# Kernel tuning notes

Measured on AMD Instinct MI355X. Metric: run time of the kernel, lower is better.

Reference implementation:

```python
import jax, jax.numpy as jnp
import numpy as np

N, E, B, D, L = 50000, 1600000, 128, 64, 5
BN_EPS = 1e-5

def _bn(x, g, b, m, v):
    # eval-mode BatchNorm1d with running stats
    return (x - m) * jax.lax.rsqrt(v + BN_EPS) * g + b

def setup_inputs() -> dict:
    key = jax.random.key(0)
    ks = iter(jax.random.split(key, 64))
    w = 1.0 / np.sqrt(D)
    def nrm(shape, s):
        return jax.random.normal(next(ks), shape, jnp.float32) * s
    def var(shape):
        return jax.random.uniform(next(ks), shape, jnp.float32) + 0.5
    inp = {
        "x": nrm((N, D), 1.0),
        "lin_W": nrm((D, D), w), "lin_b": nrm((D,), w),
        "eps": jnp.zeros((L,), jnp.float32),
        "gin_W1": nrm((L, D, D), w), "gin_b1": nrm((L, D), w),
        "gin_bn_g": jnp.ones((L, D), jnp.float32), "gin_bn_b": jnp.zeros((L, D), jnp.float32),
        "gin_bn_m": nrm((L, D), 0.1), "gin_bn_v": var((L, D)),
        "gin_W2": nrm((L, D, D), w), "gin_b2": nrm((L, D), w),
        "bn_g": jnp.ones((L, D), jnp.float32), "bn_b": jnp.zeros((L, D), jnp.float32),
        "bn_m": nrm((L, D), 0.1), "bn_v": var((L, D)),
        "vn_emb": jnp.zeros((D,), jnp.float32),  # init constant 0 per source
        "vn_W1": nrm((L - 1, D, D), w), "vn_b1": nrm((L - 1, D), w),
        "vn_bn1_g": jnp.ones((L - 1, D), jnp.float32), "vn_bn1_b": jnp.zeros((L - 1, D), jnp.float32),
        "vn_bn1_m": nrm((L - 1, D), 0.1), "vn_bn1_v": var((L - 1, D)),
        "vn_W2": nrm((L - 1, D, D), w), "vn_b2": nrm((L - 1, D), w),
        "vn_bn2_g": jnp.ones((L - 1, D), jnp.float32), "vn_bn2_b": jnp.zeros((L - 1, D), jnp.float32),
        "vn_bn2_m": nrm((L - 1, D), 0.1), "vn_bn2_v": var((L - 1, D)),
        "src": jax.random.randint(next(ks), (E,), 0, N, jnp.int32),
        "dst": jax.random.randint(next(ks), (E,), 0, N, jnp.int32),
        "batch_id": jnp.sort(jax.random.randint(next(ks), (N,), 0, B, jnp.int32)),
    }
    return inp

def reference(x, lin_W, lin_b, eps, gin_W1, gin_b1, gin_bn_g, gin_bn_b, gin_bn_m, gin_bn_v,
              gin_W2, gin_b2, bn_g, bn_b, bn_m, bn_v, vn_emb,
              vn_W1, vn_b1, vn_bn1_g, vn_bn1_b, vn_bn1_m, vn_bn1_v,
              vn_W2, vn_b2, vn_bn2_g, vn_bn2_b, vn_bn2_m, vn_bn2_v,
              src, dst, batch_id):
    n = x.shape[0]
    h = x @ lin_W + lin_b                       # input linear [N, D]
    h_list = [h]
    vn = jnp.broadcast_to(vn_emb, (B, D))       # per-graph virtual node [B, D]
    for l in range(L):
        h_list[l] = h_list[l] + vn[batch_id]    # virtual-node broadcast to nodes
        hl = h_list[l]
        # GINConv: sum over incoming edges of relu(src feature)
        agg = jax.ops.segment_sum(jax.nn.relu(hl[src]), dst, num_segments=n)
        z = (1.0 + eps[l]) * hl + agg
        z = z @ gin_W1[l] + gin_b1[l]
        z = jax.nn.relu(_bn(z, gin_bn_g[l], gin_bn_b[l], gin_bn_m[l], gin_bn_v[l]))
        z = z @ gin_W2[l] + gin_b2[l]
        z = _bn(z, bn_g[l], bn_b[l], bn_m[l], bn_v[l])  # outer batchnorm
        if l != L - 1:
            z = jax.nn.relu(z)                  # dropout is identity in eval mode
        h_list.append(z)
        if l < L - 1:
            # sum-pool nodes per graph, update virtual node via MLP
            vt = jax.ops.segment_sum(hl, batch_id, num_segments=B) + vn
            vt = vt @ vn_W1[l] + vn_b1[l]
            vt = jax.nn.relu(_bn(vt, vn_bn1_g[l], vn_bn1_b[l], vn_bn1_m[l], vn_bn1_v[l]))
            vt = vt @ vn_W2[l] + vn_b2[l]
            vn = jax.nn.relu(_bn(vt, vn_bn2_g[l], vn_bn2_b[l], vn_bn2_m[l], vn_bn2_v[l]))
    # JK='sum' in the source sums h_list[0..num_layers-1] (excludes final entry)
    out = h_list[0]
    for l in range(1, L):
        out = out + h_list[l]
    return out
```

## Files before the change

kernel.cpp:

```cpp
#include <hip/hip_runtime.h>

#define N_NODES 50000
#define N_EDGES 1600000
#define NB 128
#define GB 782
#define CAP 80
#define NODE_RANGE 6250
#define EDGE_BLOCKS 6250
#define INIT_BLOCKS 32

__device__ __forceinline__ unsigned short f2bf(float f) {
    unsigned u = __float_as_uint(f);
    unsigned r = (u + 0x7FFFu + ((u >> 16) & 1u)) >> 16;
    return (unsigned short)r;
}

__global__ __launch_bounds__(256) void k_build(
    const int* __restrict__ src, const int* __restrict__ dst,
    int* __restrict__ cnt, unsigned short* __restrict__ csr_src,
    const float* __restrict__ vn_emb, float* __restrict__ pooled) {
    int bid = blockIdx.x;
    if (bid >= EDGE_BLOCKS * 8) {
        int t = (bid - EDGE_BLOCKS * 8) * 256 + threadIdx.x;
        pooled[t] = vn_emb[t & 63];
        return;
    }
    int range = bid & 7;
    int e = (bid >> 3) * 256 + threadIdx.x;
    int d = dst[e];
    if (d / NODE_RANGE != range) return;
    int pos = atomicAdd(&cnt[d], 1);
    if (pos < CAP) csr_src[(size_t)d * CAP + pos] = (unsigned short)src[e];
}

__global__ __launch_bounds__(256) void k_lin_pre(
    const float* __restrict__ in, const float* __restrict__ W,
    const float* __restrict__ bias, const float* __restrict__ vn_emb,
    const int* __restrict__ batch_id,
    float* __restrict__ h, float* __restrict__ out,
    unsigned short* __restrict__ rbuf, float* __restrict__ pooled) {
    __shared__ float sW[64 * 64];
    __shared__ float sIn[64 * 68];
    int tid = threadIdx.x;
    int row0 = blockIdx.x * 64;

    const float4* W4 = (const float4*)W;
#pragma unroll
    for (int i = 0; i < 4; ++i) ((float4*)sW)[tid + 256 * i] = W4[tid + 256 * i];
    const float4* in4 = (const float4*)in;
#pragma unroll
    for (int i = 0; i < 4; ++i) {
        int idx = tid + 256 * i;
        int r = idx >> 4, j = idx & 15;
        float4 val = make_float4(0.f, 0.f, 0.f, 0.f);
        if (row0 + r < N_NODES) val = in4[(size_t)(row0 + r) * 16 + j];
        ((float4*)(sIn + r * 68))[j] = val;
    }
    __syncthreads();

    int c4 = (tid & 15) * 4;
    int rl = (tid >> 4) * 4;
    float acc[4][4] = {{0.f}};
#pragma unroll 8
    for (int k = 0; k < 64; ++k) {
        float4 wv = *(const float4*)(sW + k * 64 + c4);
        float a0 = sIn[(rl + 0) * 68 + k];
        float a1 = sIn[(rl + 1) * 68 + k];
        float a2 = sIn[(rl + 2) * 68 + k];
        float a3 = sIn[(rl + 3) * 68 + k];
        acc[0][0] += a0 * wv.x; acc[0][1] += a0 * wv.y; acc[0][2] += a0 * wv.z; acc[0][3] += a0 * wv.w;
        acc[1][0] += a1 * wv.x; acc[1][1] += a1 * wv.y; acc[1][2] += a1 * wv.z; acc[1][3] += a1 * wv.w;
        acc[2][0] += a2 * wv.x; acc[2][1] += a2 * wv.y; acc[2][2] += a2 * wv.z; acc[2][3] += a2 * wv.w;
        acc[3][0] += a3 * wv.x; acc[3][1] += a3 * wv.y; acc[3][2] += a3 * wv.z; acc[3][3] += a3 * wv.w;
    }
    float shf[4];
#pragma unroll
    for (int j = 0; j < 4; ++j) shf[j] = bias[c4 + j] + vn_emb[c4 + j];

    int lane = tid & 63;
    int wave = tid >> 6;
    int wr0 = row0 + wave * 16;
    bool full = (wr0 + 15 < N_NODES);
    bool fast = full && (batch_id[wr0] == batch_id[wr0 + 15]);
    float4 pacc = make_float4(0.f, 0.f, 0.f, 0.f);
#pragma unroll
    for (int r = 0; r < 4; ++r) {
        int row = row0 + rl + r;
        if (row >= N_NODES) continue;
        float4 v;
        v.x = acc[r][0] + shf[0];
        v.y = acc[r][1] + shf[1];
        v.z = acc[r][2] + shf[2];
        v.w = acc[r][3] + shf[3];
        *(float4*)(h + (size_t)row * 64 + c4) = v;
        *(float4*)(out + (size_t)row * 64 + c4) = v;
        ushort4 rb;
        rb.x = f2bf(fmaxf(v.x, 0.f)); rb.y = f2bf(fmaxf(v.y, 0.f));
        rb.z = f2bf(fmaxf(v.z, 0.f)); rb.w = f2bf(fmaxf(v.w, 0.f));
        *(ushort4*)(rbuf + (size_t)row * 64 + c4) = rb;
        if (fast) {
            pacc.x += v.x; pacc.y += v.y; pacc.z += v.z; pacc.w += v.w;
        } else {
            int b = batch_id[row];
            atomicAdd(&pooled[b * 64 + c4 + 0], v.x);
            atomicAdd(&pooled[b * 64 + c4 + 1], v.y);
            atomicAdd(&pooled[b * 64 + c4 + 2], v.z);
            atomicAdd(&pooled[b * 64 + c4 + 3], v.w);
        }
    }
    if (fast) {
        pacc.x += __shfl_xor(pacc.x, 16); pacc.x += __shfl_xor(pacc.x, 32);
        pacc.y += __shfl_xor(pacc.y, 16); pacc.y += __shfl_xor(pacc.y, 32);
        pacc.z += __shfl_xor(pacc.z, 16); pacc.z += __shfl_xor(pacc.z, 32);
        pacc.w += __shfl_xor(pacc.w, 16); pacc.w += __shfl_xor(pacc.w, 32);
        if ((lane >> 4) == 0) {
            int b = batch_id[wr0];
            atomicAdd(&pooled[b * 64 + c4 + 0], pacc.x);
            atomicAdd(&pooled[b * 64 + c4 + 1], pacc.y);
            atomicAdd(&pooled[b * 64 + c4 + 2], pacc.z);
            atomicAdd(&pooled[b * 64 + c4 + 3], pacc.w);
        }
    }
}

__global__ __launch_bounds__(512) void k_gin(
    const float* __restrict__ h_in, const float* __restrict__ eps, int l,
    const int* __restrict__ cnt, const unsigned short* __restrict__ csr_src,
    const unsigned short* __restrict__ rbuf_in,
    const float* __restrict__ W1, const float* __restrict__ b1,
    const float* __restrict__ g1, const float* __restrict__ be1,
    const float* __restrict__ m1, const float* __restrict__ v1,
    const float* __restrict__ W2, const float* __restrict__ b2,
    const float* __restrict__ g2, const float* __restrict__ be2,
    const float* __restrict__ m2, const float* __restrict__ v2,
    const float* __restrict__ vn, const int* __restrict__ batch_id,
    float* __restrict__ h, float* __restrict__ out,
    unsigned short* __restrict__ rbuf_out, float* __restrict__ pooled,
    int last) {
    __shared__ float sW[64 * 64];
    __shared__ float sIn[64 * 68];
    int tid = threadIdx.x;
    int row0 = blockIdx.x * 64;
    int lane = tid & 63;
    int wave = tid >> 6;

#pragma unroll
    for (int i = 0; i < 2; ++i)
        ((float4*)sW)[tid + 512 * i] = ((const float4*)W1)[tid + 512 * i];

    {
        int g = lane >> 3, f4 = lane & 7;
        int row = row0 + wave * 8 + g;
        float e1 = 1.0f + eps[l];
        const uint4* tab4 = (const uint4*)rbuf_in;
        float aL0 = 0.f, aH0 = 0.f, aL1 = 0.f, aH1 = 0.f;
        float aL2 = 0.f, aH2 = 0.f, aL3 = 0.f, aH3 = 0.f;
        if (row < N_NODES) {
            int deg = cnt[row]; if (deg > CAP) deg = CAP;
            const unsigned short* rowp = csr_src + (size_t)row * CAP;
            int e = 0;
            for (; e + 3 < deg; e += 4) {
                ushort4 s4 = *(const ushort4*)(rowp + e);
                uint4 u0 = tab4[(size_t)s4.x * 8 + f4];
                uint4 u1 = tab4[(size_t)s4.y * 8 + f4];
                uint4 u2 = tab4[(size_t)s4.z * 8 + f4];
                uint4 u3 = tab4[(size_t)s4.w * 8 + f4];
                aL0 += __uint_as_float(u0.x << 16); aH0 += __uint_as_float(u0.x & 0xFFFF0000u);
                aL1 += __uint_as_float(u0.y << 16); aH1 += __uint_as_float(u0.y & 0xFFFF0000u);
                aL2 += __uint_as_float(u0.z << 16); aH2 += __uint_as_float(u0.z & 0xFFFF0000u);
                aL3 += __uint_as_float(u0.w << 16); aH3 += __uint_as_float(u0.w & 0xFFFF0000u);
                aL0 += __uint_as_float(u1.x << 16); aH0 += __uint_as_float(u1.x & 0xFFFF0000u);
                aL1 += __uint_as_float(u1.y << 16); aH1 += __uint_as_float(u1.y & 0xFFFF0000u);
                aL2 += __uint_as_float(u1.z << 16); aH2 += __uint_as_float(u1.z & 0xFFFF0000u);
                aL3 += __uint_as_float(u1.w << 16); aH3 += __uint_as_float(u1.w & 0xFFFF0000u);
                aL0 += __uint_as_float(u2.x << 16); aH0 += __uint_as_float(u2.x & 0xFFFF0000u);
                aL1 += __uint_as_float(u2.y << 16); aH1 += __uint_as_float(u2.y & 0xFFFF0000u);
                aL2 += __uint_as_float(u2.z << 16); aH2 += __uint_as_float(u2.z & 0xFFFF0000u);
                aL3 += __uint_as_float(u2.w << 16); aH3 += __uint_as_float(u2.w & 0xFFFF0000u);
                aL0 += __uint_as_float(u3.x << 16); aH0 += __uint_as_float(u3.x & 0xFFFF0000u);
                aL1 += __uint_as_float(u3.y << 16); aH1 += __uint_as_float(u3.y & 0xFFFF0000u);
                aL2 += __uint_as_float(u3.z << 16); aH2 += __uint_as_float(u3.z & 0xFFFF0000u);
                aL3 += __uint_as_float(u3.w << 16); aH3 += __uint_as_float(u3.w & 0xFFFF0000u);
            }
            for (; e < deg; ++e) {
                uint4 u = tab4[(size_t)rowp[e] * 8 + f4];
                aL0 += __uint_as_float(u.x << 16); aH0 += __uint_as_float(u.x & 0xFFFF0000u);
                aL1 += __uint_as_float(u.y << 16); aH1 += __uint_as_float(u.y & 0xFFFF0000u);
                aL2 += __uint_as_float(u.z << 16); aH2 += __uint_as_float(u.z & 0xFFFF0000u);
                aL3 += __uint_as_float(u.w << 16); aH3 += __uint_as_float(u.w & 0xFFFF0000u);
            }
        }
        float* sp = sIn + (wave * 8 + g) * 68 + f4 * 8;
        if (row < N_NODES) {
            const float* hp = h_in + (size_t)row * 64 + f4 * 8;
            float4 h0 = *(const float4*)hp;
            float4 h1 = *(const float4*)(hp + 4);
            float4 o0, o1;
            o0.x = e1 * h0.x + aL0; o0.y = e1 * h0.y + aH0;
            o0.z = e1 * h0.z + aL1; o0.w = e1 * h0.w + aH1;
            o1.x = e1 * h1.x + aL2; o1.y = e1 * h1.y + aH2;
            o1.z = e1 * h1.z + aL3; o1.w = e1 * h1.w + aH3;
            *(float4*)sp = o0;
            *(float4*)(sp + 4) = o1;
        } else {
            *(float4*)sp = make_float4(0.f, 0.f, 0.f, 0.f);
            *(float4*)(sp + 4) = make_float4(0.f, 0.f, 0.f, 0.f);
        }
    }
    __syncthreads();

    int c4 = (tid & 15) * 4;
    int rg = tid >> 4;
    float acc[2][4] = {{0.f}};
#pragma unroll 8
    for (int k = 0; k < 64; ++k) {
        float4 wv = *(const float4*)(sW + k * 64 + c4);
        float a0 = sIn[(2 * rg + 0) * 68 + k];
        float a1 = sIn[(2 * rg + 1) * 68 + k];
        acc[0][0] += a0 * wv.x; acc[0][1] += a0 * wv.y; acc[0][2] += a0 * wv.z; acc[0][3] += a0 * wv.w;
        acc[1][0] += a1 * wv.x; acc[1][1] += a1 * wv.y; acc[1][2] += a1 * wv.z; acc[1][3] += a1 * wv.w;
    }
    float scl[4], shf[4];
#pragma unroll
    for (int j = 0; j < 4; ++j) {
        int c = c4 + j;
        float sc = g1[c] * rsqrtf(v1[c] + 1e-5f);
        scl[j] = sc;
        shf[j] = be1[c] - m1[c] * sc + b1[c] * sc;
    }
    __syncthreads();
#pragma unroll
    for (int i = 0; i < 2; ++i) {
        float4 z;
        z.x = fmaxf(acc[i][0] * scl[0] + shf[0], 0.f);
        z.y = fmaxf(acc[i][1] * scl[1] + shf[1], 0.f);
        z.z = fmaxf(acc[i][2] * scl[2] + shf[2], 0.f);
        z.w = fmaxf(acc[i][3] * scl[3] + shf[3], 0.f);
        *(float4*)(sIn + (2 * rg + i) * 68 + c4) = z;
    }
#pragma unroll
    for (int i = 0; i < 2; ++i)
        ((float4*)sW)[tid + 512 * i] = ((const float4*)W2)[tid + 512 * i];
    __syncthreads();

    float acc2[2][4] = {{0.f}};
#pragma unroll 8
    for (int k = 0; k < 64; ++k) {
        float4 wv = *(const float4*)(sW + k * 64 + c4);
        float a0 = sIn[(2 * rg + 0) * 68 + k];
        float a1 = sIn[(2 * rg + 1) * 68 + k];
        acc2[0][0] += a0 * wv.x; acc2[0][1] += a0 * wv.y; acc2[0][2] += a0 * wv.z; acc2[0][3] += a0 * wv.w;
        acc2[1][0] += a1 * wv.x; acc2[1][1] += a1 * wv.y; acc2[1][2] += a1 * wv.z; acc2[1][3] += a1 * wv.w;
    }
#pragma unroll
    for (int j = 0; j < 4; ++j) {
        int c = c4 + j;
        float sc = g2[c] * rsqrtf(v2[c] + 1e-5f);
        scl[j] = sc;
        shf[j] = be2[c] - m2[c] * sc + b2[c] * sc;
    }

    int wr0 = row0 + wave * 8;
    bool full = (wr0 + 7 < N_NODES);
    bool fast = (!last) && full && (batch_id[wr0] == batch_id[wr0 + 7]);
    float4 pacc = make_float4(0.f, 0.f, 0.f, 0.f);
#pragma unroll
    for (int r = 0; r < 2; ++r) {
        int row = row0 + rg * 2 + r;
        if (row >= N_NODES) continue;
        int b = batch_id[row];
        float4 vv = *(const float4*)(vn + b * 64 + c4);
        float4 v;
        v.x = fmaxf(acc2[r][0] * scl[0] + shf[0], 0.f) + vv.x;
        v.y = fmaxf(acc2[r][1] * scl[1] + shf[1], 0.f) + vv.y;
        v.z = fmaxf(acc2[r][2] * scl[2] + shf[2], 0.f) + vv.z;
        v.w = fmaxf(acc2[r][3] * scl[3] + shf[3], 0.f) + vv.w;
        float4 o = *(const float4*)(out + (size_t)row * 64 + c4);
        o.x += v.x; o.y += v.y; o.z += v.z; o.w += v.w;
        *(float4*)(out + (size_t)row * 64 + c4) = o;
        if (!last) {
            *(float4*)(h + (size_t)row * 64 + c4) = v;
            ushort4 rb;
            rb.x = f2bf(fmaxf(v.x, 0.f)); rb.y = f2bf(fmaxf(v.y, 0.f));
            rb.z = f2bf(fmaxf(v.z, 0.f)); rb.w = f2bf(fmaxf(v.w, 0.f));
            *(ushort4*)(rbuf_out + (size_t)row * 64 + c4) = rb;
            if (fast) {
                pacc.x += v.x; pacc.y += v.y; pacc.z += v.z; pacc.w += v.w;
            } else {
                atomicAdd(&pooled[b * 64 + c4 + 0], v.x);
                atomicAdd(&pooled[b * 64 + c4 + 1], v.y);
                atomicAdd(&pooled[b * 64 + c4 + 2], v.z);
                atomicAdd(&pooled[b * 64 + c4 + 3], v.w);
            }
        }
    }
    if (fast) {
        pacc.x += __shfl_xor(pacc.x, 16); pacc.x += __shfl_xor(pacc.x, 32);
        pacc.y += __shfl_xor(pacc.y, 16); pacc.y += __shfl_xor(pacc.y, 32);
        pacc.z += __shfl_xor(pacc.z, 16); pacc.z += __shfl_xor(pacc.z, 32);
        pacc.w += __shfl_xor(pacc.w, 16); pacc.w += __shfl_xor(pacc.w, 32);
        if ((lane >> 4) == 0) {
            int b = batch_id[wr0];
            atomicAdd(&pooled[b * 64 + c4 + 0], pacc.x);
            atomicAdd(&pooled[b * 64 + c4 + 1], pacc.y);
            atomicAdd(&pooled[b * 64 + c4 + 2], pacc.z);
            atomicAdd(&pooled[b * 64 + c4 + 3], pacc.w);
        }
    }
}

__global__ __launch_bounds__(1024) void k_vnmlp(
    const float* __restrict__ pooled_in,
    const float* __restrict__ W1, const float* __restrict__ b1,
    const float* __restrict__ g1, const float* __restrict__ be1,
    const float* __restrict__ m1, const float* __restrict__ v1,
    const float* __restrict__ W2, const float* __restrict__ b2,
    const float* __restrict__ g2, const float* __restrict__ be2,
    const float* __restrict__ m2, const float* __restrict__ v2,
    float* __restrict__ vn_out, float* __restrict__ pooled_out) {
    __shared__ float sP[128 * 68];
    __shared__ float sW[64 * 64];
    int tid = threadIdx.x;

    ((float4*)sW)[tid] = ((const float4*)W1)[tid];
#pragma unroll
    for (int i = 0; i < 2; ++i) {
        int idx = tid + 1024 * i;
        int r = idx >> 4, j = idx & 15;
        ((float4*)(sP + r * 68))[j] = ((const float4*)pooled_in)[idx];
    }
    __syncthreads();

    int c4 = (tid & 15) * 4, rg = tid >> 4;
    float acc[2][4] = {{0.f}};
#pragma unroll 8
    for (int k = 0; k < 64; ++k) {
        float4 w = *(const float4*)(sW + k * 64 + c4);
#pragma unroll
        for (int i = 0; i < 2; ++i) {
            float a = sP[(rg * 2 + i) * 68 + k];
            acc[i][0] += a * w.x; acc[i][1] += a * w.y;
            acc[i][2] += a * w.z; acc[i][3] += a * w.w;
        }
    }
    float scl[4], shf[4];
#pragma unroll
    for (int j = 0; j < 4; ++j) {
        int c = c4 + j;
        float sc = g1[c] * rsqrtf(v1[c] + 1e-5f);
        scl[j] = sc;
        shf[j] = be1[c] - m1[c] * sc + b1[c] * sc;
    }
    __syncthreads();
#pragma unroll
    for (int i = 0; i < 2; ++i) {
        float4 z;
        z.x = fmaxf(acc[i][0] * scl[0] + shf[0], 0.f);
        z.y = fmaxf(acc[i][1] * scl[1] + shf[1], 0.f);
        z.z = fmaxf(acc[i][2] * scl[2] + shf[2], 0.f);
        z.w = fmaxf(acc[i][3] * scl[3] + shf[3], 0.f);
        *(float4*)(sP + (rg * 2 + i) * 68 + c4) = z;
    }
    ((float4*)sW)[tid] = ((const float4*)W2)[tid];
    __syncthreads();

    float acc2[2][4] = {{0.f}};
#pragma unroll 8
    for (int k = 0; k < 64; ++k) {
        float4 w = *(const float4*)(sW + k * 64 + c4);
#pragma unroll
        for (int i = 0; i < 2; ++i) {
            float a = sP[(rg * 2 + i) * 68 + k];
            acc2[i][0] += a * w.x; acc2[i][1] += a * w.y;
            acc2[i][2] += a * w.z; acc2[i][3] += a * w.w;
        }
    }
#pragma unroll
    for (int j = 0; j < 4; ++j) {
        int c = c4 + j;
        float sc = g2[c] * rsqrtf(v2[c] + 1e-5f);
        scl[j] = sc;
        shf[j] = be2[c] - m2[c] * sc + b2[c] * sc;
    }
#pragma unroll
    for (int i = 0; i < 2; ++i) {
        int row = rg * 2 + i;
        float4 o;
        o.x = fmaxf(acc2[i][0] * scl[0] + shf[0], 0.f);
        o.y = fmaxf(acc2[i][1] * scl[1] + shf[1], 0.f);
        o.z = fmaxf(acc2[i][2] * scl[2] + shf[2], 0.f);
        o.w = fmaxf(acc2[i][3] * scl[3] + shf[3], 0.f);
        *(float4*)(vn_out + row * 64 + c4) = o;
        *(float4*)(pooled_out + row * 64 + c4) = o;
    }
}

extern "C" void kernel_launch(void* const* d_in, const int* in_sizes, int n_in,
                              void* d_out, int out_size, void* d_ws, size_t ws_size,
                              hipStream_t stream) {
    const float* x      = (const float*)d_in[0];
    const float* lin_W  = (const float*)d_in[1];
    const float* lin_b  = (const float*)d_in[2];
    const float* eps    = (const float*)d_in[3];
    const float* gin_W1 = (const float*)d_in[4];
    const float* gin_b1 = (const float*)d_in[5];
    const float* gbn_g  = (const float*)d_in[6];
    const float* gbn_b  = (const float*)d_in[7];
    const float* gbn_m  = (const float*)d_in[8];
    const float* gbn_v  = (const float*)d_in[9];
    const float* gin_W2 = (const float*)d_in[10];
    const float* gin_b2 = (const float*)d_in[11];
    const float* bn_g   = (const float*)d_in[12];
    const float* bn_b   = (const float*)d_in[13];
    const float* bn_m   = (const float*)d_in[14];
    const float* bn_v   = (const float*)d_in[15];
    const float* vn_emb = (const float*)d_in[16];
    const float* vn_W1  = (const float*)d_in[17];
    const float* vn_b1  = (const float*)d_in[18];
    const float* v1g    = (const float*)d_in[19];
    const float* v1b    = (const float*)d_in[20];
    const float* v1m    = (const float*)d_in[21];
    const float* v1v    = (const float*)d_in[22];
    const float* vn_W2  = (const float*)d_in[23];
    const float* vn_b2  = (const float*)d_in[24];
    const float* v2g    = (const float*)d_in[25];
    const float* v2b    = (const float*)d_in[26];
    const float* v2m    = (const float*)d_in[27];
    const float* v2v    = (const float*)d_in[28];
    const int* src      = (const int*)d_in[29];
    const int* dst      = (const int*)d_in[30];
    const int* batch_id = (const int*)d_in[31];
    float* out = (float*)d_out;

    float* h      = (float*)d_ws;
    unsigned short* rbufA = (unsigned short*)(h + (size_t)N_NODES * 64);
    unsigned short* rbufB = rbufA + (size_t)N_NODES * 64;
    float* vn     = (float*)(rbufB + (size_t)N_NODES * 64);
    float* pooled = vn  + (size_t)NB * 64;
    int*   cnt    = (int*)(pooled + (size_t)NB * 64);
    unsigned short* csr_src = (unsigned short*)(cnt + N_NODES);

    hipMemsetAsync(cnt, 0, N_NODES * sizeof(int), stream);
    k_build<<<EDGE_BLOCKS * 8 + INIT_BLOCKS, 256, 0, stream>>>(src, dst, cnt, csr_src,
                                                               vn_emb, pooled);

    k_lin_pre<<<GB, 256, 0, stream>>>(x, lin_W, lin_b, vn_emb, batch_id,
                                      h, out, rbufA, pooled);

    for (int l = 0; l < 4; ++l) {
        unsigned short* rin  = (l & 1) ? rbufB : rbufA;
        unsigned short* rout = (l & 1) ? rbufA : rbufB;
        k_vnmlp<<<1, 1024, 0, stream>>>(pooled,
                                        vn_W1 + l * 4096, vn_b1 + l * 64,
                                        v1g + l * 64, v1b + l * 64, v1m + l * 64, v1v + l * 64,
                                        vn_W2 + l * 4096, vn_b2 + l * 64,
                                        v2g + l * 64, v2b + l * 64, v2m + l * 64, v2v + l * 64,
                                        vn, pooled);
        k_gin<<<GB, 512, 0, stream>>>(h, eps, l, cnt, csr_src, rin,
                                      gin_W1 + l * 4096, gin_b1 + l * 64,
                                      gbn_g + l * 64, gbn_b + l * 64,
                                      gbn_m + l * 64, gbn_v + l * 64,
                                      gin_W2 + l * 4096, gin_b2 + l * 64,
                                      bn_g + l * 64, bn_b + l * 64,
                                      bn_m + l * 64, bn_v + l * 64,
                                      vn, batch_id, h, out, rout, pooled,
                                      l == 3);
    }
}
```

Baseline: 485.1 us.

## Split bf16 gather table into two feature halves gathered in separate kernels

Stores the relu'd bf16 node table as two planar halves of 32 features each. A new kernel gathers and sums the first half into a float buffer, and the fused GIN kernel then gathers only the second half and reads the first half back from that buffer. The aim is to make each gather pass's random-access working set (3.2 MB per half) fit better in cache. The cost is an extra kernel launch per layer, an extra round trip for the intermediate buffer, and reading the CSR indices twice.

```diff
diff --git a/kernel.cpp b/kernel.cpp
--- a/kernel.cpp
+++ b/kernel.cpp
@@ -14,6 +14,8 @@
     unsigned r = (u + 0x7FFFu + ((u >> 16) & 1u)) >> 16;
     return (unsigned short)r;
 }
+__device__ __forceinline__ float bflo(unsigned u) { return __uint_as_float(u << 16); }
+__device__ __forceinline__ float bfhi(unsigned u) { return __uint_as_float(u & 0xFFFF0000u); }
 
 __global__ __launch_bounds__(256) void k_build(
     const int* __restrict__ src, const int* __restrict__ dst,
@@ -97,7 +99,8 @@
         ushort4 rb;
         rb.x = f2bf(fmaxf(v.x, 0.f)); rb.y = f2bf(fmaxf(v.y, 0.f));
         rb.z = f2bf(fmaxf(v.z, 0.f)); rb.w = f2bf(fmaxf(v.w, 0.f));
-        *(ushort4*)(rbuf + (size_t)row * 64 + c4) = rb;
+        *(ushort4*)(rbuf + (size_t)(c4 >> 5) * ((size_t)N_NODES * 32)
+                    + (size_t)row * 32 + (c4 & 31)) = rb;
         if (fast) {
             pacc.x += v.x; pacc.y += v.y; pacc.z += v.z; pacc.w += v.w;
         } else {
@@ -123,10 +126,47 @@
     }
 }
 
+__global__ __launch_bounds__(512) void k_gath(
+    const float* __restrict__ h_in, const float* __restrict__ eps, int l,
+    const int* __restrict__ cnt, const unsigned short* __restrict__ csr_src,
+    const unsigned short* __restrict__ rbuf_in, float* __restrict__ agg0) {
+    int tid = threadIdx.x;
+    int lane = tid & 63, wave = tid >> 6;
+    int g = lane >> 3, f = lane & 7;
+    int row = blockIdx.x * 64 + wave * 8 + g;
+    if (row >= N_NODES) return;
+    float e1 = 1.0f + eps[l];
+    const uint2* tab = (const uint2*)rbuf_in;
+    float a0 = 0.f, a1 = 0.f, a2 = 0.f, a3 = 0.f;
+    int deg = cnt[row]; if (deg > CAP) deg = CAP;
+    const unsigned short* rowp = csr_src + (size_t)row * CAP;
+    int e = 0;
+    for (; e + 3 < deg; e += 4) {
+        ushort4 s4 = *(const ushort4*)(rowp + e);
+        uint2 u0 = tab[(size_t)s4.x * 8 + f];
+        uint2 u1 = tab[(size_t)s4.y * 8 + f];
+        uint2 u2 = tab[(size_t)s4.z * 8 + f];
+        uint2 u3 = tab[(size_t)s4.w * 8 + f];
+        a0 += bflo(u0.x); a1 += bfhi(u0.x); a2 += bflo(u0.y); a3 += bfhi(u0.y);
+        a0 += bflo(u1.x); a1 += bfhi(u1.x); a2 += bflo(u1.y); a3 += bfhi(u1.y);
+        a0 += bflo(u2.x); a1 += bfhi(u2.x); a2 += bflo(u2.y); a3 += bfhi(u2.y);
+        a0 += bflo(u3.x); a1 += bfhi(u3.x); a2 += bflo(u3.y); a3 += bfhi(u3.y);
+    }
+    for (; e < deg; ++e) {
+        uint2 u = tab[(size_t)rowp[e] * 8 + f];
+        a0 += bflo(u.x); a1 += bfhi(u.x); a2 += bflo(u.y); a3 += bfhi(u.y);
+    }
+    float4 hv = *(const float4*)(h_in + (size_t)row * 64 + 4 * f);
+    float4 o;
+    o.x = e1 * hv.x + a0; o.y = e1 * hv.y + a1;
+    o.z = e1 * hv.z + a2; o.w = e1 * hv.w + a3;
+    *(float4*)(agg0 + (size_t)row * 32 + 4 * f) = o;
+}
+
 __global__ __launch_bounds__(512) void k_gin(
     const float* __restrict__ h_in, const float* __restrict__ eps, int l,
     const int* __restrict__ cnt, const unsigned short* __restrict__ csr_src,
-    const unsigned short* __restrict__ rbuf_in,
+    const unsigned short* __restrict__ rbuf_in, const float* __restrict__ agg0,
     const float* __restrict__ W1, const float* __restrict__ b1,
     const float* __restrict__ g1, const float* __restrict__ be1,
     const float* __restrict__ m1, const float* __restrict__ v1,
@@ -149,62 +189,48 @@
         ((float4*)sW)[tid + 512 * i] = ((const float4*)W1)[tid + 512 * i];
 
     {
-        int g = lane >> 3, f4 = lane & 7;
+        int r = tid >> 3, j = tid & 7;
+        int row = row0 + r;
+        float4 val = make_float4(0.f, 0.f, 0.f, 0.f);
+        if (row < N_NODES) val = *(const float4*)(agg0 + (size_t)row * 32 + j * 4);
+        *(float4*)(sIn + r * 68 + j * 4) = val;
+    }
+
+    {
+        int g = lane >> 3, f = lane & 7;
         int row = row0 + wave * 8 + g;
         float e1 = 1.0f + eps[l];
-        const uint4* tab4 = (const uint4*)rbuf_in;
-        float aL0 = 0.f, aH0 = 0.f, aL1 = 0.f, aH1 = 0.f;
-        float aL2 = 0.f, aH2 = 0.f, aL3 = 0.f, aH3 = 0.f;
+        const uint2* tab = (const uint2*)(rbuf_in + (size_t)N_NODES * 32);
+        float a0 = 0.f, a1 = 0.f, a2 = 0.f, a3 = 0.f;
         if (row < N_NODES) {
             int deg = cnt[row]; if (deg > CAP) deg = CAP;
             const unsigned short* rowp = csr_src + (size_t)row * CAP;
             int e = 0;
             for (; e + 3 < deg; e += 4) {
                 ushort4 s4 = *(const ushort4*)(rowp + e);
-                uint4 u0 = tab4[(size_t)s4.x * 8 + f4];
-                uint4 u1 = tab4[(size_t)s4.y * 8 + f4];
-                uint4 u2 = tab4[(size_t)s4.z * 8 + f4];
-                uint4 u3 = tab4[(size_t)s4.w * 8 + f4];
-                aL0 += __uint_as_float(u0.x << 16); aH0 += __uint_as_float(u0.x & 0xFFFF0000u);
-                aL1 += __uint_as_float(u0.y << 16); aH1 += __uint_as_float(u0.y & 0xFFFF0000u);
-                aL2 += __uint_as_float(u0.z << 16); aH2 += __uint_as_float(u0.z & 0xFFFF0000u);
-                aL3 += __uint_as_float(u0.w << 16); aH3 += __uint_as_float(u0.w & 0xFFFF0000u);
-                aL0 += __uint_as_float(u1.x << 16); aH0 += __uint_as_float(u1.x & 0xFFFF0000u);
-                aL1 += __uint_as_float(u1.y << 16); aH1 += __uint_as_float(u1.y & 0xFFFF0000u);
-                aL2 += __uint_as_float(u1.z << 16); aH2 += __uint_as_float(u1.z & 0xFFFF0000u);
-                aL3 += __uint_as_float(u1.w << 16); aH3 += __uint_as_float(u1.w & 0xFFFF0000u);
-                aL0 += __uint_as_float(u2.x << 16); aH0 += __uint_as_float(u2.x & 0xFFFF0000u);
-                aL1 += __uint_as_float(u2.y << 16); aH1 += __uint_as_float(u2.y & 0xFFFF0000u);
-                aL2 += __uint_as_float(u2.z << 16); aH2 += __uint_as_float(u2.z & 0xFFFF0000u);
-                aL3 += __uint_as_float(u2.w << 16); aH3 += __uint_as_float(u2.w & 0xFFFF0000u);
-                aL0 += __uint_as_float(u3.x << 16); aH0 += __uint_as_float(u3.x & 0xFFFF0000u);
-                aL1 += __uint_as_float(u3.y << 16); aH1 += __uint_as_float(u3.y & 0xFFFF0000u);
-                aL2 += __uint_as_float(u3.z << 16); aH2 += __uint_as_float(u3.z & 0xFFFF0000u);
-                aL3 += __uint_as_float(u3.w << 16); aH3 += __uint_as_float(u3.w & 0xFFFF0000u);
+                uint2 u0 = tab[(size_t)s4.x * 8 + f];
+                uint2 u1 = tab[(size_t)s4.y * 8 + f];
+                uint2 u2 = tab[(size_t)s4.z * 8 + f];
+                uint2 u3 = tab[(size_t)s4.w * 8 + f];
+                a0 += bflo(u0.x); a1 += bfhi(u0.x); a2 += bflo(u0.y); a3 += bfhi(u0.y);
+                a0 += bflo(u1.x); a1 += bfhi(u1.x); a2 += bflo(u1.y); a3 += bfhi(u1.y);
+                a0 += bflo(u2.x); a1 += bfhi(u2.x); a2 += bflo(u2.y); a3 += bfhi(u2.y);
+                a0 += bflo(u3.x); a1 += bfhi(u3.x); a2 += bflo(u3.y); a3 += bfhi(u3.y);
             }
             for (; e < deg; ++e) {
-                uint4 u = tab4[(size_t)rowp[e] * 8 + f4];
-                aL0 += __uint_as_float(u.x << 16); aH0 += __uint_as_float(u.x & 0xFFFF0000u);
-                aL1 += __uint_as_float(u.y << 16); aH1 += __uint_as_float(u.y & 0xFFFF0000u);
-                aL2 += __uint_as_float(u.z << 16); aH2 += __uint_as_float(u.z & 0xFFFF0000u);
-                aL3 += __uint_as_float(u.w << 16); aH3 += __uint_as_float(u.w & 0xFFFF0000u);
+                uint2 u = tab[(size_t)rowp[e] * 8 + f];
+                a0 += bflo(u.x); a1 += bfhi(u.x); a2 += bflo(u.y); a3 += bfhi(u.y);
             }
         }
-        float* sp = sIn + (wave * 8 + g) * 68 + f4 * 8;
+        float* sp = sIn + (wave * 8 + g) * 68 + 32 + 4 * f;
         if (row < N_NODES) {
-            const float* hp = h_in + (size_t)row * 64 + f4 * 8;
-            float4 h0 = *(const float4*)hp;
-            float4 h1 = *(const float4*)(hp + 4);
-            float4 o0, o1;
-            o0.x = e1 * h0.x + aL0; o0.y = e1 * h0.y + aH0;
-            o0.z = e1 * h0.z + aL1; o0.w = e1 * h0.w + aH1;
-            o1.x = e1 * h1.x + aL2; o1.y = e1 * h1.y + aH2;
-            o1.z = e1 * h1.z + aL3; o1.w = e1 * h1.w + aH3;
-            *(float4*)sp = o0;
-            *(float4*)(sp + 4) = o1;
+            float4 hv = *(const float4*)(h_in + (size_t)row * 64 + 32 + 4 * f);
+            float4 o;
+            o.x = e1 * hv.x + a0; o.y = e1 * hv.y + a1;
+            o.z = e1 * hv.z + a2; o.w = e1 * hv.w + a3;
+            *(float4*)sp = o;
         } else {
             *(float4*)sp = make_float4(0.f, 0.f, 0.f, 0.f);
-            *(float4*)(sp + 4) = make_float4(0.f, 0.f, 0.f, 0.f);
         }
     }
     __syncthreads();
@@ -283,7 +309,8 @@
             ushort4 rb;
             rb.x = f2bf(fmaxf(v.x, 0.f)); rb.y = f2bf(fmaxf(v.y, 0.f));
             rb.z = f2bf(fmaxf(v.z, 0.f)); rb.w = f2bf(fmaxf(v.w, 0.f));
-            *(ushort4*)(rbuf_out + (size_t)row * 64 + c4) = rb;
+            *(ushort4*)(rbuf_out + (size_t)(c4 >> 5) * ((size_t)N_NODES * 32)
+                        + (size_t)row * 32 + (c4 & 31)) = rb;
             if (fast) {
                 pacc.x += v.x; pacc.y += v.y; pacc.z += v.z; pacc.w += v.w;
             } else {
@@ -435,7 +462,8 @@
     float* h      = (float*)d_ws;
     unsigned short* rbufA = (unsigned short*)(h + (size_t)N_NODES * 64);
     unsigned short* rbufB = rbufA + (size_t)N_NODES * 64;
-    float* vn     = (float*)(rbufB + (size_t)N_NODES * 64);
+    float* agg0   = (float*)(rbufB + (size_t)N_NODES * 64);
+    float* vn     = agg0 + (size_t)N_NODES * 32;
     float* pooled = vn  + (size_t)NB * 64;
     int*   cnt    = (int*)(pooled + (size_t)NB * 64);
     unsigned short* csr_src = (unsigned short*)(cnt + N_NODES);
@@ -456,7 +484,8 @@
                                         vn_W2 + l * 4096, vn_b2 + l * 64,
                                         v2g + l * 64, v2b + l * 64, v2m + l * 64, v2v + l * 64,
                                         vn, pooled);
-        k_gin<<<GB, 512, 0, stream>>>(h, eps, l, cnt, csr_src, rin,
+        k_gath<<<GB, 512, 0, stream>>>(h, eps, l, cnt, csr_src, rin, agg0);
+        k_gin<<<GB, 512, 0, stream>>>(h, eps, l, cnt, csr_src, rin, agg0,
                                       gin_W1 + l * 4096, gin_b1 + l * 64,
                                       gbn_g + l * 64, gbn_b + l * 64,
                                       gbn_m + l * 64, gbn_v + l * 64,
```

New measurement: 551.8 us. 13.8% more time.
